# Kernel tuning notes

Measured on AMD Instinct MI355X. Metric: run time of the kernel, lower is better.

## Reference

```python
import jax, jax.numpy as jnp
import numpy as np

VOCAB, P, K, B, L, R = 50257, 512, 64, 32, 2048, 5


def setup_inputs() -> dict:
    key = jax.random.key(0)
    k1, k2, k3, k4, k5, k6, k7 = jax.random.split(key, 7)
    return {
        "x": jax.random.randint(k1, (B, L), 0, VOCAB, dtype=jnp.int32),
        "V": jax.random.normal(k2, (VOCAB, P), dtype=jnp.float32),
        "C": jax.random.normal(k3, (K, P), dtype=jnp.float32),
        "f1_w": jax.random.normal(k4, (2 * R + 1,), dtype=jnp.float32),
        "f1_b": jax.random.normal(k5, (K,), dtype=jnp.float32),
        "f2_w": jax.random.normal(k6, (K, P), dtype=jnp.float32),
        "f2_b": jax.random.normal(k7, (K,), dtype=jnp.float32),
    }


def reference(x, V, C, f1_w, f1_b, f2_w, f2_b):
    b, l = x.shape
    k, p = C.shape
    w = f1_w.shape[0]
    r = (w - 1) // 2
    emb = V[x]                                              # [B,L,P] embedding lookup
    x_hat = emb / jnp.linalg.norm(emb, axis=2, keepdims=True)
    l_hat = C / jnp.linalg.norm(C, axis=1, keepdims=True)
    G = jnp.einsum('kp,blp->bkl', l_hat, x_hat)             # cosine sim [B,K,L]
    # sliding-window dot product == depthwise 1D cross-correlation, 'same' padding
    u = jax.lax.conv_general_dilated(
        G.reshape(b * k, 1, l), f1_w.reshape(1, 1, w),
        window_strides=(1,), padding=[(r, r)],
        dimension_numbers=('NCH', 'OIH', 'NCH'),
    ).reshape(b, k, l)
    m = jax.nn.relu(u + f1_b[None, :, None])                # [B,K,L]
    beta = jax.nn.softmax(m.max(axis=1), axis=1)            # max over labels, softmax over seq -> [B,L]
    pooled = jnp.mean(beta[:, :, None] * emb, axis=1)       # [B,P]
    return pooled @ f2_w.T + f2_b                           # [B,K]
```

## Files before the change

kernel.cpp:

```cpp
#include <hip/hip_runtime.h>
#include <hip/hip_bf16.h>

#define PP     512
#define KK     64
#define BB     32
#define LLEN   2048
#define TPOS   64
#define SROWS  74
#define NCHUNK (LLEN / TPOS)
#define CPB    4

typedef __attribute__((ext_vector_type(8)))  short short8;
typedef __attribute__((ext_vector_type(16))) float float16;

__device__ inline unsigned int pack_bf2(float lo, float hi) {
    __hip_bfloat162 h = __float22bfloat162_rn(make_float2(lo, hi));
    unsigned int u;
    __builtin_memcpy(&u, &h, 4);
    return u;
}
__device__ inline float bf_lo(unsigned int v) { return __uint_as_float(v << 16); }
__device__ inline float bf_hi(unsigned int v) { return __uint_as_float(v & 0xffff0000u); }

__global__ void k1_prep(const float* __restrict__ C, const float* __restrict__ f2w,
                        ushort* __restrict__ Bu) {
    const int n = blockIdx.x;
    const float* src = (n < 64) ? (C + n * PP) : (f2w + (n - 64) * PP);
    const int t = threadIdx.x;
    float v0 = src[t];
    float v1 = src[t + 256];
    __shared__ float red[256];
    red[t] = v0 * v0 + v1 * v1;
    __syncthreads();
    for (int s = 128; s > 0; s >>= 1) {
        if (t < s) red[t] += red[t + s];
        __syncthreads();
    }
    const float inv = (n < 64) ? rsqrtf(red[0]) : 1.f;
    Bu[(((t >> 3)       * 128 + n) << 3) + (t & 7)] = (ushort)(pack_bf2(v0 * inv, 0.f) & 0xffffu);
    Bu[((((t + 256) >> 3)) * 128 + n) * 8 + (t & 7)] = (ushort)(pack_bf2(v1 * inv, 0.f) & 0xffffu);
}

__launch_bounds__(512, 2)
__global__ void k2_fused(const int* __restrict__ x, const float* __restrict__ V,
                         const uint4* __restrict__ Bu4,
                         const float* __restrict__ f1w, const float* __restrict__ f1b,
                         float* __restrict__ pool) {
    __shared__ uint4 sA[2][SROWS * 64];
    __shared__ int   stok[2][SROWS];
    __shared__ float rnorm[2][SROWS];
    __shared__ float smv[TPOS];
    __shared__ float sp[TPOS];
    __shared__ float sscal[2];

    const int tid  = threadIdx.x;
    const int lane = tid & 63;
    const int wv   = tid >> 6;
    const int l31  = lane & 31;
    const int chunk0 = blockIdx.x * CPB;

    const int o   = tid & 7;
    const int r   = tid >> 3;
    const int ht  = tid - 352;
    const int h16 = ht & 15;
    const int rh  = 64 + (ht >> 4);

    float4 pa[8], pb[8], ph[8];

    const int rowBase = (wv == 0) ? 0 : (wv == 1) ? 32 : (wv == 2) ? 42
                      : (wv == 3) ? 5 : 37;
    const int cc = lane >> 5;

    float w[11];
#pragma unroll
    for (int t = 0; t < 11; ++t) w[t] = f1w[t];
    const int j = l31;
    const int h = tid >> 5;
    const float bias0 = f1b[j], bias1 = f1b[j + 32];

    auto LOADTOK = [&](int bi, int chunk) {
        if (tid < SROWS) {
            const int bb = chunk >> 5;
            const int l0 = (chunk & 31) * TPOS;
            int gl = min(max(l0 - 5 + tid, 0), LLEN - 1);
            stok[bi][tid] = x[bb * LLEN + gl];
        }
    };
    auto ISSUE = [&](int bi) {
        const float4* f4 = (const float4*)(V + (size_t)stok[bi][r] * PP);
#pragma unroll
        for (int g = 0; g < 8; ++g) pa[g] = f4[o + g * 8];
#pragma unroll
        for (int g = 0; g < 8; ++g) pb[g] = f4[o + (g + 8) * 8];
        if (ht >= 0) {
            const float4* f4h = (const float4*)(V + (size_t)stok[bi][rh] * PP);
#pragma unroll
            for (int g = 0; g < 8; ++g) ph[g] = f4h[h16 + g * 16];
        }
    };
    auto PACK = [&](int bi) {
        const int swzr = r & 7;
        float nrm = 0.f;
#pragma unroll
        for (int g = 0; g < 8; ++g) {
            const float4 a = pa[g];
            nrm = fmaf(a.x, a.x, fmaf(a.y, a.y, fmaf(a.z, a.z, fmaf(a.w, a.w, nrm))));
            uint2 w2; w2.x = pack_bf2(a.x, a.y); w2.y = pack_bf2(a.z, a.w);
            const int f = g * 4 + (o >> 1);
            ((uint2*)&sA[bi][r * 64 + (f ^ swzr)])[o & 1] = w2;
        }
#pragma unroll
        for (int g = 0; g < 8; ++g) {
            const float4 a = pb[g];
            nrm = fmaf(a.x, a.x, fmaf(a.y, a.y, fmaf(a.z, a.z, fmaf(a.w, a.w, nrm))));
            uint2 w2; w2.x = pack_bf2(a.x, a.y); w2.y = pack_bf2(a.z, a.w);
            const int f = (g + 8) * 4 + (o >> 1);
            ((uint2*)&sA[bi][r * 64 + (f ^ swzr)])[o & 1] = w2;
        }
        nrm += __shfl_xor(nrm, 1, 64);
        nrm += __shfl_xor(nrm, 2, 64);
        nrm += __shfl_xor(nrm, 4, 64);
        if (o == 0) rnorm[bi][r] = rsqrtf(nrm);
        if (ht >= 0) {
            const int swzh = rh & 7;
            float nh2 = 0.f;
#pragma unroll
            for (int g = 0; g < 8; ++g) {
                const float4 a = ph[g];
                nh2 = fmaf(a.x, a.x, fmaf(a.y, a.y, fmaf(a.z, a.z, fmaf(a.w, a.w, nh2))));
                uint2 w2; w2.x = pack_bf2(a.x, a.y); w2.y = pack_bf2(a.z, a.w);
                const int f = g * 8 + (h16 >> 1);
                ((uint2*)&sA[bi][rh * 64 + (f ^ swzh)])[h16 & 1] = w2;
            }
            nh2 += __shfl_xor(nh2, 1, 64);
            nh2 += __shfl_xor(nh2, 2, 64);
            nh2 += __shfl_xor(nh2, 4, 64);
            nh2 += __shfl_xor(nh2, 8, 64);
            if (h16 == 0) rnorm[bi][rh] = rsqrtf(nh2);
        }
    };

    int cur = 0;
    LOADTOK(0, chunk0);
    __syncthreads();
    ISSUE(0);
    PACK(0);

#pragma unroll 1
    for (int i = 0; i < CPB; ++i) {
        const int chunk = chunk0 + i;
        const int l0 = (chunk & 31) * TPOS;
        const int nxt = cur ^ 1;

        if (i + 1 < CPB) LOADTOK(nxt, chunk + 1);
        __syncthreads();

        if (i + 1 < CPB) ISSUE(nxt);
        __builtin_amdgcn_sched_barrier(0);

        float16 c0, c1;
#pragma unroll
        for (int k = 0; k < 16; ++k) { c0[k] = 0.f; c1[k] = 0.f; }
        if (wv < 5) {
            const int nh    = (wv < 3) ? 0 : 64;
            const int row   = rowBase + l31;
            const int abase = row * 64;
            const int aswz  = row & 7;
#pragma unroll 8
            for (int ks = 0; ks < 32; ++ks) {
                const int ff = ks * 2 + cc;
                const uint4 av = sA[cur][abase + (ff ^ aswz)];
                const uint4 b0 = Bu4[ff * 128 + nh + l31];
                const uint4 b1 = Bu4[ff * 128 + nh + 32 + l31];
                short8 a8, t0, t1;
                __builtin_memcpy(&a8, &av, 16);
                __builtin_memcpy(&t0, &b0, 16);
                __builtin_memcpy(&t1, &b1, 16);
                c0 = __builtin_amdgcn_mfma_f32_32x32x16_bf16(a8, t0, c0, 0, 0, 0);
                c1 = __builtin_amdgcn_mfma_f32_32x32x16_bf16(a8, t1, c1, 0, 0, 0);
            }
        }
        __builtin_amdgcn_sched_barrier(0);
        __syncthreads();

        if (i + 1 < CPB) PACK(nxt);

        unsigned int* G32 = (unsigned int*)&sA[cur][0];
        float*        E2s = (float*)((char*)&sA[cur][0] + 10240);
        float*        sred = (float*)((char*)&sA[cur][0] + 28672);
        if (wv < 3) {
#pragma unroll
            for (int reg = 0; reg < 16; ++reg) {
                const int rr  = (reg & 3) + 8 * (reg >> 2) + 4 * cc;
                const int row = rowBase + rr;
                if (wv == 2 && row < 64) continue;
                const int gl = l0 - 5 + row;
                unsigned int vpk = 0u;
                if (gl >= 0 && gl < LLEN) {
                    const float rn = rnorm[cur][row];
                    vpk = pack_bf2(c0[reg] * rn, c1[reg] * rn);
                }
                G32[row * 32 + l31] = vpk;
            }
        } else if (wv < 5) {
#pragma unroll
            for (int reg = 0; reg < 16; ++reg) {
                const int rr = (reg & 3) + 8 * (reg >> 2) + 4 * cc;
                const int oo = rowBase - 5 + rr;
                E2s[oo * 64 + l31]      = c0[reg];
                E2s[oo * 64 + 32 + l31] = c1[reg];
            }
        }
        __syncthreads();

#pragma unroll
        for (int it = 0; it < 4; ++it) {
            const int oo = it * 16 + h;
            float u0 = 0.f, u1 = 0.f;
#pragma unroll
            for (int tap = 0; tap < 11; ++tap) {
                const unsigned int v = G32[(oo + tap) * 32 + j];
                u0 = fmaf(bf_lo(v), w[tap], u0);
                u1 = fmaf(bf_hi(v), w[tap], u1);
            }
            float m = fmaxf(fmaxf(u0 + bias0, 0.f), fmaxf(u1 + bias1, 0.f));
#pragma unroll
            for (int off = 16; off > 0; off >>= 1)
                m = fmaxf(m, __shfl_xor(m, off, 64));
            if (j == 0) smv[oo] = m;
        }
        __syncthreads();

        if (tid < 64) {
            float v = smv[tid];
#pragma unroll
            for (int off = 32; off > 0; off >>= 1)
                v = fmaxf(v, __shfl_xor(v, off, 64));
            if (tid == 0) sscal[0] = v;
        }
        __syncthreads();
        const float mx = sscal[0];
        if (tid < 64) sp[tid] = __expf(smv[tid] - mx);
        __syncthreads();
        if (tid < 64) {
            float s = sp[tid];
#pragma unroll
            for (int off = 32; off > 0; off >>= 1)
                s += __shfl_xor(s, off, 64);
            if (tid == 0) sscal[1] = s;
        }

        float a0 = 0.f, a1 = 0.f;
#pragma unroll
        for (int it = 0; it < 4; ++it) {
            const int oo = it * 16 + h;
            const float wgt = sp[oo];
            a0 = fmaf(wgt, E2s[oo * 64 + j], a0);
            a1 = fmaf(wgt, E2s[oo * 64 + 32 + j], a1);
        }
        __syncthreads();
        sred[h * 64 + j]      = a0;
        sred[h * 64 + j + 32] = a1;
        __syncthreads();
        if (tid < 64) {
            float rr = 0.f;
#pragma unroll
            for (int hh = 0; hh < 16; ++hh) rr += sred[hh * 64 + tid];
            float* dst = pool + (size_t)chunk * 68;
            dst[tid] = rr;
            if (tid == 0) { dst[64] = sscal[0]; dst[65] = sscal[1]; }
        }
        __syncthreads();
        cur ^= 1;
    }
}

__global__ void k6_final(const float* __restrict__ pool, const float* __restrict__ f2b,
                         float* __restrict__ out) {
    const int b = blockIdx.x;
    const int k = threadIdx.x;
    float M = -1e30f;
#pragma unroll
    for (int c = 0; c < NCHUNK; ++c)
        M = fmaxf(M, pool[(size_t)(b * NCHUNK + c) * 68 + 64]);
    float tot = 0.f, num = 0.f;
#pragma unroll
    for (int c = 0; c < NCHUNK; ++c) {
        const float* pc = pool + (size_t)(b * NCHUNK + c) * 68;
        const float sc = __expf(pc[64] - M);
        tot = fmaf(sc, pc[65], tot);
        num = fmaf(sc, pc[k], num);
    }
    out[b * KK + k] = (num / tot) * (1.f / 2048.f) + f2b[k];
}

extern "C" void kernel_launch(void* const* d_in, const int* in_sizes, int n_in,
                              void* d_out, int out_size, void* d_ws, size_t ws_size,
                              hipStream_t stream) {
    const int*   x   = (const int*)d_in[0];
    const float* V   = (const float*)d_in[1];
    const float* C   = (const float*)d_in[2];
    const float* f1w = (const float*)d_in[3];
    const float* f1b = (const float*)d_in[4];
    const float* f2w = (const float*)d_in[5];
    const float* f2b = (const float*)d_in[6];
    float* out = (float*)d_out;

    float* ws = (float*)d_ws;
    ushort* Bu = (ushort*)ws;
    float* pool = ws + 32768;

    k1_prep <<<128, 256, 0, stream>>>(C, f2w, Bu);
    k2_fused<<<(BB * NCHUNK) / CPB, 512, 0, stream>>>(x, V, (const uint4*)Bu, f1w, f1b, pool);
    k6_final<<<BB, 64, 0, stream>>>(pool, f2b, out);
}
```

Measured before the change: 207.9 us.

## Single-buffer LDS and halve chunks per block to raise occupancy

Removes the double-buffered shared staging (sA, stok, rnorm) in favor of a single buffer, reads token ids directly from global memory instead of staging them in LDS, and halves chunks per block so twice as many blocks launch. Launch bounds ask for four blocks of 512 threads per CU instead of two. The aim is more resident waves to hide embedding-gather latency, in place of software double-buffering. The prefetch of the next chunk's rows into registers still overlaps the MFMA loop, but PACK now sits on the critical path before each compute, and the tighter register budget may cause spills.

```diff
diff --git a/kernel.cpp b/kernel.cpp
--- a/kernel.cpp
+++ b/kernel.cpp
@@ -8,7 +8,7 @@
 #define TPOS   64
 #define SROWS  74
 #define NCHUNK (LLEN / TPOS)
-#define CPB    4
+#define CPB    2
 
 typedef __attribute__((ext_vector_type(8)))  short short8;
 typedef __attribute__((ext_vector_type(16))) float float16;
@@ -41,14 +41,13 @@
     Bu[((((t + 256) >> 3)) * 128 + n) * 8 + (t & 7)] = (ushort)(pack_bf2(v1 * inv, 0.f) & 0xffffu);
 }
 
-__launch_bounds__(512, 2)
+__launch_bounds__(512, 4)
 __global__ void k2_fused(const int* __restrict__ x, const float* __restrict__ V,
                          const uint4* __restrict__ Bu4,
                          const float* __restrict__ f1w, const float* __restrict__ f1b,
                          float* __restrict__ pool) {
-    __shared__ uint4 sA[2][SROWS * 64];
-    __shared__ int   stok[2][SROWS];
-    __shared__ float rnorm[2][SROWS];
+    __shared__ uint4 sA[SROWS * 64];
+    __shared__ float rnorm[SROWS];
     __shared__ float smv[TPOS];
     __shared__ float sp[TPOS];
     __shared__ float sscal[2];
@@ -78,27 +77,25 @@
     const int h = tid >> 5;
     const float bias0 = f1b[j], bias1 = f1b[j + 32];
 
-    auto LOADTOK = [&](int bi, int chunk) {
-        if (tid < SROWS) {
-            const int bb = chunk >> 5;
-            const int l0 = (chunk & 31) * TPOS;
-            int gl = min(max(l0 - 5 + tid, 0), LLEN - 1);
-            stok[bi][tid] = x[bb * LLEN + gl];
-        }
-    };
-    auto ISSUE = [&](int bi) {
-        const float4* f4 = (const float4*)(V + (size_t)stok[bi][r] * PP);
+    auto ISSUE = [&](int chunk) {
+        const int bb = chunk >> 5;
+        const int l0c = (chunk & 31) * TPOS;
+        const int gl  = min(max(l0c - 5 + r, 0), LLEN - 1);
+        const int tok = x[bb * LLEN + gl];
+        const float4* f4 = (const float4*)(V + (size_t)tok * PP);
 #pragma unroll
         for (int g = 0; g < 8; ++g) pa[g] = f4[o + g * 8];
 #pragma unroll
         for (int g = 0; g < 8; ++g) pb[g] = f4[o + (g + 8) * 8];
         if (ht >= 0) {
-            const float4* f4h = (const float4*)(V + (size_t)stok[bi][rh] * PP);
+            const int glh  = min(max(l0c - 5 + rh, 0), LLEN - 1);
+            const int tokh = x[bb * LLEN + glh];
+            const float4* f4h = (const float4*)(V + (size_t)tokh * PP);
 #pragma unroll
             for (int g = 0; g < 8; ++g) ph[g] = f4h[h16 + g * 16];
         }
     };
-    auto PACK = [&](int bi) {
+    auto PACK = [&]() {
         const int swzr = r & 7;
         float nrm = 0.f;
 #pragma unroll
@@ -107,7 +104,7 @@
             nrm = fmaf(a.x, a.x, fmaf(a.y, a.y, fmaf(a.z, a.z, fmaf(a.w, a.w, nrm))));
             uint2 w2; w2.x = pack_bf2(a.x, a.y); w2.y = pack_bf2(a.z, a.w);
             const int f = g * 4 + (o >> 1);
-            ((uint2*)&sA[bi][r * 64 + (f ^ swzr)])[o & 1] = w2;
+            ((uint2*)&sA[r * 64 + (f ^ swzr)])[o & 1] = w2;
         }
 #pragma unroll
         for (int g = 0; g < 8; ++g) {
@@ -115,12 +112,12 @@
             nrm = fmaf(a.x, a.x, fmaf(a.y, a.y, fmaf(a.z, a.z, fmaf(a.w, a.w, nrm))));
             uint2 w2; w2.x = pack_bf2(a.x, a.y); w2.y = pack_bf2(a.z, a.w);
             const int f = (g + 8) * 4 + (o >> 1);
-            ((uint2*)&sA[bi][r * 64 + (f ^ swzr)])[o & 1] = w2;
+            ((uint2*)&sA[r * 64 + (f ^ swzr)])[o & 1] = w2;
         }
         nrm += __shfl_xor(nrm, 1, 64);
         nrm += __shfl_xor(nrm, 2, 64);
         nrm += __shfl_xor(nrm, 4, 64);
-        if (o == 0) rnorm[bi][r] = rsqrtf(nrm);
+        if (o == 0) rnorm[r] = rsqrtf(nrm);
         if (ht >= 0) {
             const int swzh = rh & 7;
             float nh2 = 0.f;
@@ -130,32 +127,27 @@
                 nh2 = fmaf(a.x, a.x, fmaf(a.y, a.y, fmaf(a.z, a.z, fmaf(a.w, a.w, nh2))));
                 uint2 w2; w2.x = pack_bf2(a.x, a.y); w2.y = pack_bf2(a.z, a.w);
                 const int f = g * 8 + (h16 >> 1);
-                ((uint2*)&sA[bi][rh * 64 + (f ^ swzh)])[h16 & 1] = w2;
+                ((uint2*)&sA[rh * 64 + (f ^ swzh)])[h16 & 1] = w2;
             }
             nh2 += __shfl_xor(nh2, 1, 64);
             nh2 += __shfl_xor(nh2, 2, 64);
             nh2 += __shfl_xor(nh2, 4, 64);
             nh2 += __shfl_xor(nh2, 8, 64);
-            if (h16 == 0) rnorm[bi][rh] = rsqrtf(nh2);
+            if (h16 == 0) rnorm[rh] = rsqrtf(nh2);
         }
     };
 
-    int cur = 0;
-    LOADTOK(0, chunk0);
-    __syncthreads();
-    ISSUE(0);
-    PACK(0);
-
-#pragma unroll 1
+    ISSUE(chunk0);
+
+#pragma unroll
     for (int i = 0; i < CPB; ++i) {
         const int chunk = chunk0 + i;
         const int l0 = (chunk & 31) * TPOS;
-        const int nxt = cur ^ 1;
-
-        if (i + 1 < CPB) LOADTOK(nxt, chunk + 1);
-        __syncthreads();
-
-        if (i + 1 < CPB) ISSUE(nxt);
+
+        PACK();
+        __syncthreads();
+
+        if (i + 1 < CPB) ISSUE(chunk + 1);
         __builtin_amdgcn_sched_barrier(0);
 
         float16 c0, c1;
@@ -169,7 +161,7 @@
 #pragma unroll 8
             for (int ks = 0; ks < 32; ++ks) {
                 const int ff = ks * 2 + cc;
-                const uint4 av = sA[cur][abase + (ff ^ aswz)];
+                const uint4 av = sA[abase + (ff ^ aswz)];
                 const uint4 b0 = Bu4[ff * 128 + nh + l31];
                 const uint4 b1 = Bu4[ff * 128 + nh + 32 + l31];
                 short8 a8, t0, t1;
@@ -183,11 +175,9 @@
         __builtin_amdgcn_sched_barrier(0);
         __syncthreads();
 
-        if (i + 1 < CPB) PACK(nxt);
-
-        unsigned int* G32 = (unsigned int*)&sA[cur][0];
-        float*        E2s = (float*)((char*)&sA[cur][0] + 10240);
-        float*        sred = (float*)((char*)&sA[cur][0] + 28672);
+        unsigned int* G32 = (unsigned int*)sA;
+        float*        E2s = (float*)((char*)sA + 10240);
+        float*        sred = (float*)((char*)sA + 28672);
         if (wv < 3) {
 #pragma unroll
             for (int reg = 0; reg < 16; ++reg) {
@@ -197,7 +187,7 @@
                 const int gl = l0 - 5 + row;
                 unsigned int vpk = 0u;
                 if (gl >= 0 && gl < LLEN) {
-                    const float rn = rnorm[cur][row];
+                    const float rn = rnorm[row];
                     vpk = pack_bf2(c0[reg] * rn, c1[reg] * rn);
                 }
                 G32[row * 32 + l31] = vpk;
@@ -271,7 +261,6 @@
             if (tid == 0) { dst[64] = sscal[0]; dst[65] = sscal[1]; }
         }
         __syncthreads();
-        cur ^= 1;
     }
 }
 
```

After: 237.9 us. 1.14x slower.
